# Optimization experiments

Measured on AMD Instinct MI355X. Metric: run time of the kernel, lower is better.

The kernel has to match this reference:

```python
import jax, jax.numpy as jnp
import numpy as np

DIM = 512
HEADS = 8
HEAD_DIM = DIM // HEADS
K = 16
SCALE = HEAD_DIM ** -0.5
EPS = 1e-5


def _layer_norm(x, g, b):
    mu = jnp.mean(x, axis=-1, keepdims=True)
    var = jnp.mean(jnp.square(x - mu), axis=-1, keepdims=True)
    return (x - mu) * jax.lax.rsqrt(var + EPS) * g + b


def setup_inputs() -> dict:
    key = jax.random.key(0)
    ks = jax.random.split(key, 16)
    D = DIM
    s = D ** -0.5
    x = jax.random.normal(ks[0], (2, 4096, D), dtype=jnp.float32)
    p = {
        'x': x,
        'q_w': jax.random.normal(ks[1], (D, D), jnp.float32) * s,
        'q_b': jnp.zeros((D,), jnp.float32),
        'k_w': jax.random.normal(ks[2], (D, D), jnp.float32) * s,
        'k_b': jnp.zeros((D,), jnp.float32),
        'v_w': jax.random.normal(ks[3], (D, D), jnp.float32) * s,
        'v_b': jnp.zeros((D,), jnp.float32),
        'o_w': jax.random.normal(ks[4], (D, D), jnp.float32) * s,
        'o_b': jnp.zeros((D,), jnp.float32),
        'ln1_g': jnp.ones((D,), jnp.float32),
        'ln1_b': jnp.zeros((D,), jnp.float32),
        'ln2_g': jnp.ones((D,), jnp.float32),
        'ln2_b': jnp.zeros((D,), jnp.float32),
        'ff1_w': jax.random.normal(ks[5], (D, 4 * D), jnp.float32) * s,
        'ff1_b': jnp.zeros((4 * D,), jnp.float32),
        'ff2_w': jax.random.normal(ks[6], (4 * D, D), jnp.float32) * (4 * D) ** -0.5,
        'ff2_b': jnp.zeros((D,), jnp.float32),
    }
    return p


def reference(x, q_w, q_b, k_w, k_b, v_w, v_b, o_w, o_b,
              ln1_g, ln1_b, ln2_g, ln2_b, ff1_w, ff1_b, ff2_w, ff2_b):
    B, N, D = x.shape
    residual = x
    xn = _layer_norm(x, ln1_g, ln1_b)
    Q = (xn @ q_w + q_b).reshape(B, N, HEADS, HEAD_DIM)
    Kt = (xn @ k_w + k_b).reshape(B, N, HEADS, HEAD_DIM)
    V = (xn @ v_w + v_b).reshape(B, N, HEADS, HEAD_DIM)
    # dense scores [B,H,N,N]
    logits = jnp.einsum('bnhd,bmhd->bhnm', Q, Kt) * SCALE
    topk_vals, topk_idx = jax.lax.top_k(logits, K)  # [B,H,N,K]
    # softmax over only the top-k entries == scatter(-inf) + dense softmax
    attn = jax.nn.softmax(topk_vals, axis=-1)
    Vh = V.transpose(0, 2, 1, 3)  # [B,H,M,hd]
    # gather V rows at top-k indices -> [B,H,N,K,hd]
    Vg = jnp.take_along_axis(Vh[:, :, None, :, :], topk_idx[..., None], axis=3)
    out = jnp.einsum('bhnk,bhnkd->bnhd', attn, Vg).reshape(B, N, D)
    out = out @ o_w + o_b
    x2 = residual + out
    h = _layer_norm(x2, ln2_g, ln2_b)
    ff = jax.nn.gelu(h @ ff1_w + ff1_b, approximate=False) @ ff2_w + ff2_b
    return x2 + ff
```

## Files before the change

### kernel.cpp

```cpp
#include <hip/hip_runtime.h>
#include <math.h>

#define DIMD 512
#define NSEQ 4096
#define NHEAD 8
#define HD 64
#define TOPK 16

__global__ __launch_bounds__(256) void ln_stats_kernel(
    const float* __restrict__ X, float2* __restrict__ S)
{
    int r = blockIdx.x;
    int t = threadIdx.x;
    const float* xr = X + (size_t)r * DIMD;
    float a = xr[t], b = xr[t + 256];
    float s = a + b;
    float sq = a * a + b * b;
    #pragma unroll
    for (int off = 32; off > 0; off >>= 1) {
        s  += __shfl_down(s, off, 64);
        sq += __shfl_down(sq, off, 64);
    }
    __shared__ float red[8];
    int wv = t >> 6, ln = t & 63;
    if (ln == 0) { red[wv] = s; red[wv + 4] = sq; }
    __syncthreads();
    if (t == 0) {
        float st  = red[0] + red[1] + red[2] + red[3];
        float sqt = red[4] + red[5] + red[6] + red[7];
        float mean = st * (1.0f / DIMD);
        float var  = sqt * (1.0f / DIMD) - mean * mean;
        float inv  = 1.0f / sqrtf(var + 1e-5f);
        S[r] = make_float2(mean, inv);
    }
}

__global__ __launch_bounds__(256) void gemm_f32(
    const float* __restrict__ A, const float* __restrict__ W,
    const float* __restrict__ bias, const float* __restrict__ R,
    float* __restrict__ C, int Kd, int Nn, int gelu,
    const float2* __restrict__ lnstats,
    const float* __restrict__ lng, const float* __restrict__ lnb)
{
    __shared__ float As[32][64];
    __shared__ float Ws[32][64];
    int n0 = blockIdx.x * 64;
    int m0 = blockIdx.y * 64;
    int t  = threadIdx.x;
    int tr = t >> 4, tc = t & 15;
    float acc[4][4] = {};

    for (int k0 = 0; k0 < Kd; k0 += 32) {
        #pragma unroll
        for (int qq = 0; qq < 2; ++qq) {
            int idx = t * 2 + qq;
            int r   = idx >> 3;
            int c4  = idx & 7;
            float4 av = *(const float4*)&A[(size_t)(m0 + r) * Kd + k0 + c4 * 4];
            if (lnstats) {
                float2 st = lnstats[m0 + r];
                float4 gv = *(const float4*)&lng[k0 + c4 * 4];
                float4 bv = *(const float4*)&lnb[k0 + c4 * 4];
                av.x = (av.x - st.x) * st.y * gv.x + bv.x;
                av.y = (av.y - st.x) * st.y * gv.y + bv.y;
                av.z = (av.z - st.x) * st.y * gv.z + bv.z;
                av.w = (av.w - st.x) * st.y * gv.w + bv.w;
            }
            As[c4 * 4 + 0][r] = av.x;
            As[c4 * 4 + 1][r] = av.y;
            As[c4 * 4 + 2][r] = av.z;
            As[c4 * 4 + 3][r] = av.w;
            int kr  = idx >> 4;
            int nc4 = idx & 15;
            *(float4*)&Ws[kr][nc4 * 4] =
                *(const float4*)&W[(size_t)(k0 + kr) * Nn + n0 + nc4 * 4];
        }
        __syncthreads();
        #pragma unroll
        for (int kk = 0; kk < 32; ++kk) {
            float4 a = *(const float4*)&As[kk][tr * 4];
            float4 b = *(const float4*)&Ws[kk][tc * 4];
            acc[0][0] += a.x * b.x; acc[0][1] += a.x * b.y;
            acc[0][2] += a.x * b.z; acc[0][3] += a.x * b.w;
            acc[1][0] += a.y * b.x; acc[1][1] += a.y * b.y;
            acc[1][2] += a.y * b.z; acc[1][3] += a.y * b.w;
            acc[2][0] += a.z * b.x; acc[2][1] += a.z * b.y;
            acc[2][2] += a.z * b.z; acc[2][3] += a.z * b.w;
            acc[3][0] += a.w * b.x; acc[3][1] += a.w * b.y;
            acc[3][2] += a.w * b.z; acc[3][3] += a.w * b.w;
        }
        __syncthreads();
    }

    float4 bb = *(const float4*)&bias[n0 + tc * 4];
    #pragma unroll
    for (int i = 0; i < 4; ++i) {
        int row = m0 + tr * 4 + i;
        float4 o;
        o.x = acc[i][0] + bb.x;
        o.y = acc[i][1] + bb.y;
        o.z = acc[i][2] + bb.z;
        o.w = acc[i][3] + bb.w;
        if (gelu) {
            o.x = 0.5f * o.x * (1.0f + erff(o.x * 0.70710678118654752f));
            o.y = 0.5f * o.y * (1.0f + erff(o.y * 0.70710678118654752f));
            o.z = 0.5f * o.z * (1.0f + erff(o.z * 0.70710678118654752f));
            o.w = 0.5f * o.w * (1.0f + erff(o.w * 0.70710678118654752f));
        }
        if (R) {
            float4 rv = *(const float4*)&R[(size_t)row * Nn + n0 + tc * 4];
            o.x += rv.x; o.y += rv.y; o.z += rv.z; o.w += rv.w;
        }
        *(float4*)&C[(size_t)row * Nn + n0 + tc * 4] = o;
    }
}

#define INSERT_SLOT(SLOTV, SLOTI)                                        \
    {                                                                    \
        unsigned long long lt = __ballot(SLOTV < scb);                   \
        int cnt = __popcll((lt >> (gg * 16)) & 0xFFFFull);               \
        if (cnt) {                                                       \
            float shv = __shfl(SLOTV, (lane + 1) & 63);                  \
            int   shi = __shfl(SLOTI, (lane + 1) & 63);                  \
            bool put = ing && (s == cnt - 1);                            \
            bool shf = ing && (s < cnt - 1);                             \
            SLOTV = put ? scb : (shf ? shv : SLOTV);                     \
            SLOTI = put ? idxb : (shf ? shi : SLOTI);                    \
        }                                                                \
    }

__global__ __launch_bounds__(512, 2) void topk_attn_fused(
    const float* __restrict__ Qm, const float* __restrict__ Km,
    const float* __restrict__ Vm, float* __restrict__ Om)
{
    __shared__ float4 Ks4[64 * 16];

    int bid = blockIdx.x;
    int bh  = bid >> 6;
    int qt  = bid & 63;
    int b   = bh >> 3, h = bh & 7;
    int qbase = qt * 64;
    int tid  = threadIdx.x;
    int wid  = __builtin_amdgcn_readfirstlane(tid >> 6);
    int lane = tid & 63;
    int grp  = lane >> 4;
    int s    = lane & 15;

    size_t kbase = ((size_t)b * NSEQ) * DIMD + h * HD;
    const float* qrow0 = Qm + ((size_t)(b * NSEQ + qbase + wid * 8)) * DIMD + h * HD;

    float slotvA = -INFINITY, slotvB = -INFINITY;
    int   slotiA = 0,         slotiB = 0;

    for (int t0 = 0; t0 < NSEQ; t0 += 64) {
        __syncthreads();
        #pragma unroll
        for (int qq = 0; qq < 2; ++qq) {
            int idx = tid * 2 + qq;
            int r   = idx >> 4;
            int c4  = idx & 15;
            Ks4[r * 16 + (c4 ^ (r & 15))] =
                *(const float4*)&Km[kbase + (size_t)(t0 + r) * DIMD + c4 * 4];
        }
        __syncthreads();

        float4 kr[16];
        #pragma unroll
        for (int d4 = 0; d4 < 16; ++d4)
            kr[d4] = Ks4[lane * 16 + (d4 ^ (lane & 15))];

        #pragma unroll
        for (int g = 0; g < 8; ++g) {
            const float* qrow = qrow0 + (size_t)g * DIMD;
            float a0 = 0.f, a1 = 0.f, a2 = 0.f, a3 = 0.f;
            #pragma unroll
            for (int d4 = 0; d4 < 16; ++d4) {
                float4 qv = *(const float4*)(qrow + d4 * 4);
                a0 = fmaf(qv.x, kr[d4].x, a0);
                a1 = fmaf(qv.y, kr[d4].y, a1);
                a2 = fmaf(qv.z, kr[d4].z, a2);
                a3 = fmaf(qv.w, kr[d4].w, a3);
            }
            float sc = ((a0 + a1) + (a2 + a3)) * 0.125f;

            int gg = g & 3;
            bool ing = (grp == gg);
            float theta = __shfl((g < 4) ? slotvA : slotvB, gg * 16);
            unsigned long long cand = __ballot(sc > theta);
            while (cand) {
                int src = __ffsll(cand) - 1;
                cand &= cand - 1;
                float scb  = __shfl(sc, src);
                int   idxb = t0 + src;
                if (g < 4) INSERT_SLOT(slotvA, slotiA)
                else       INSERT_SLOT(slotvB, slotiB)
            }
        }
    }

    #pragma unroll
    for (int set = 0; set < 2; ++set) {
        float slotv = set ? slotvB : slotvA;
        int   sloti = set ? slotiB : slotiA;
        float mx = __shfl(slotv, (lane & 48) + 15);
        float w  = expf(slotv - mx);
        float ssum = w;
        #pragma unroll
        for (int off = 1; off < 16; off <<= 1) ssum += __shfl_xor(ssum, off);
        float wn = w * (1.0f / ssum);

        #pragma unroll
        for (int gg2 = 0; gg2 < 4; ++gg2) {
            float acc = 0.f;
            #pragma unroll
            for (int i = 15; i >= 0; --i) {
                float wi = __shfl(wn, gg2 * 16 + i);
                int   ki = __shfl(sloti, gg2 * 16 + i);
                acc = fmaf(wi, Vm[((size_t)(b * NSEQ + ki)) * DIMD + h * HD + lane], acc);
            }
            int qn = qbase + wid * 8 + set * 4 + gg2;
            Om[((size_t)(b * NSEQ + qn)) * DIMD + h * HD + lane] = acc;
        }
    }
}

extern "C" void kernel_launch(void* const* d_in, const int* in_sizes, int n_in,
                              void* d_out, int out_size, void* d_ws, size_t ws_size,
                              hipStream_t stream)
{
    (void)in_sizes; (void)n_in; (void)out_size; (void)ws_size;
    const float* x    = (const float*)d_in[0];
    const float* q_w  = (const float*)d_in[1];
    const float* q_b  = (const float*)d_in[2];
    const float* k_w  = (const float*)d_in[3];
    const float* k_b  = (const float*)d_in[4];
    const float* v_w  = (const float*)d_in[5];
    const float* v_b  = (const float*)d_in[6];
    const float* o_w  = (const float*)d_in[7];
    const float* o_b  = (const float*)d_in[8];
    const float* ln1g = (const float*)d_in[9];
    const float* ln1b = (const float*)d_in[10];
    const float* ln2g = (const float*)d_in[11];
    const float* ln2b = (const float*)d_in[12];
    const float* ff1w = (const float*)d_in[13];
    const float* ff1b = (const float*)d_in[14];
    const float* ff2w = (const float*)d_in[15];
    const float* ff2b = (const float*)d_in[16];
    float* out = (float*)d_out;
    float* ws  = (float*)d_ws;

    const size_t SZ = (size_t)8192 * DIMD;
    float*  Qb      = ws;
    float*  Kb      = ws + SZ;
    float*  Vb      = ws + 2 * SZ;
    float*  attnOut = ws + 3 * SZ;
    float2* stats   = (float2*)(ws + 4 * SZ);
    float*  ffb     = ws;

    dim3 g512(8, 128);

    ln_stats_kernel<<<8192, 256, 0, stream>>>(x, stats);
    gemm_f32<<<g512, 256, 0, stream>>>(x, q_w, q_b, nullptr, Qb,
                                       512, 512, 0, stats, ln1g, ln1b);
    gemm_f32<<<g512, 256, 0, stream>>>(x, k_w, k_b, nullptr, Kb,
                                       512, 512, 0, stats, ln1g, ln1b);
    gemm_f32<<<g512, 256, 0, stream>>>(x, v_w, v_b, nullptr, Vb,
                                       512, 512, 0, stats, ln1g, ln1b);

    topk_attn_fused<<<1024, 512, 0, stream>>>(Qb, Kb, Vb, attnOut);

    gemm_f32<<<g512, 256, 0, stream>>>(attnOut, o_w, o_b, x, out,
                                       512, 512, 0, nullptr, nullptr, nullptr);

    ln_stats_kernel<<<8192, 256, 0, stream>>>(out, stats);
    gemm_f32<<<dim3(32, 128), 256, 0, stream>>>(out, ff1w, ff1b, nullptr, ffb,
                                                512, 2048, 1, stats, ln2g, ln2b);
    gemm_f32<<<g512, 256, 0, stream>>>(ffb, ff2w, ff2b, out, out,
                                       2048, 512, 0, nullptr, nullptr, nullptr);
}
```

Measured before the change: 2.091 ms.

## Stage Q tile in LDS and restructure score loop for higher occupancy

Loads the block's 64 query rows into shared memory once, so per-tile global/uniform Q loads go away. The score loop becomes outer-over-d4, inner-over-8-queries, keeping 32 accumulators instead of 16 float4 K registers. Launch bounds are raised to 4 blocks per SM to improve occupancy. This adds LDS broadcast reads of Q each tile and adds register pressure under the tighter bound.

```diff
diff --git a/kernel.cpp b/kernel.cpp
--- a/kernel.cpp
+++ b/kernel.cpp
@@ -129,11 +129,12 @@
         }                                                                \
     }
 
-__global__ __launch_bounds__(512, 2) void topk_attn_fused(
+__global__ __launch_bounds__(512, 4) void topk_attn_fused(
     const float* __restrict__ Qm, const float* __restrict__ Km,
     const float* __restrict__ Vm, float* __restrict__ Om)
 {
     __shared__ float4 Ks4[64 * 16];
+    __shared__ float4 Qs4[64 * 16];
 
     int bid = blockIdx.x;
     int bh  = bid >> 6;
@@ -147,7 +148,15 @@
     int s    = lane & 15;
 
     size_t kbase = ((size_t)b * NSEQ) * DIMD + h * HD;
-    const float* qrow0 = Qm + ((size_t)(b * NSEQ + qbase + wid * 8)) * DIMD + h * HD;
+
+    #pragma unroll
+    for (int qq = 0; qq < 2; ++qq) {
+        int idx = tid * 2 + qq;
+        int r   = idx >> 4;
+        int c4  = idx & 15;
+        Qs4[r * 16 + c4] = *(const float4*)
+            &Qm[((size_t)(b * NSEQ + qbase + r)) * DIMD + h * HD + c4 * 4];
+    }
 
     float slotvA = -INFINITY, slotvB = -INFINITY;
     int   slotiA = 0,         slotiB = 0;
@@ -164,25 +173,25 @@
         }
         __syncthreads();
 
-        float4 kr[16];
-        #pragma unroll
-        for (int d4 = 0; d4 < 16; ++d4)
-            kr[d4] = Ks4[lane * 16 + (d4 ^ (lane & 15))];
+        float a0[8], a1[8], a2[8], a3[8];
+        #pragma unroll
+        for (int g = 0; g < 8; ++g) { a0[g] = a1[g] = a2[g] = a3[g] = 0.f; }
+        #pragma unroll 4
+        for (int d4 = 0; d4 < 16; ++d4) {
+            float4 kv = Ks4[lane * 16 + (d4 ^ (lane & 15))];
+            #pragma unroll
+            for (int g = 0; g < 8; ++g) {
+                float4 qv = Qs4[(wid * 8 + g) * 16 + d4];
+                a0[g] = fmaf(qv.x, kv.x, a0[g]);
+                a1[g] = fmaf(qv.y, kv.y, a1[g]);
+                a2[g] = fmaf(qv.z, kv.z, a2[g]);
+                a3[g] = fmaf(qv.w, kv.w, a3[g]);
+            }
+        }
 
         #pragma unroll
         for (int g = 0; g < 8; ++g) {
-            const float* qrow = qrow0 + (size_t)g * DIMD;
-            float a0 = 0.f, a1 = 0.f, a2 = 0.f, a3 = 0.f;
-            #pragma unroll
-            for (int d4 = 0; d4 < 16; ++d4) {
-                float4 qv = *(const float4*)(qrow + d4 * 4);
-                a0 = fmaf(qv.x, kr[d4].x, a0);
-                a1 = fmaf(qv.y, kr[d4].y, a1);
-                a2 = fmaf(qv.z, kr[d4].z, a2);
-                a3 = fmaf(qv.w, kr[d4].w, a3);
-            }
-            float sc = ((a0 + a1) + (a2 + a3)) * 0.125f;
-
+            float sc = ((a0[g] + a1[g]) + (a2[g] + a3[g])) * 0.125f;
             int gg = g & 3;
             bool ing = (grp == gg);
             float theta = __shfl((g < 4) ? slotvA : slotvB, gg * 16);
```

New measurement: 1.967 ms. 1.06x faster.
